# Optimization experiments

Hardware: AMD Instinct MI355X
Metric: run time of the kernel (lower is better)

Reference implementation:

```python
import jax, jax.numpy as jnp
import numpy as np

B, L, D, H, F, NL = 8, 1024, 640, 10, 1280, 6
DH = D // H
WINDOW = 64  # spatial-neighbor band half-width
NEG = -1e9


def layer_norm(x, g, b, eps=1e-5):
    m = jnp.mean(x, axis=-1, keepdims=True)
    v = jnp.mean((x - m) ** 2, axis=-1, keepdims=True)
    return (x - m) * jax.lax.rsqrt(v + eps) * g + b


def setup_inputs() -> dict:
    key = jax.random.key(0)
    ks = jax.random.split(key, 20)
    s = 0.02
    x = jax.random.normal(ks[0], (B, L, D), jnp.float32)
    y = jax.random.normal(ks[1], (B, L, D), jnp.float32)
    idx = jnp.arange(L)
    band = jnp.abs(idx[:, None] - idx[None, :]) > WINDOW  # True = disallowed
    x_attn_mask = jnp.broadcast_to(band, (B, L, L))
    y_attn_mask = jnp.broadcast_to(band, (B, L, L))
    x_pad_mask = jnp.zeros((B, L), bool)
    y_pad_mask = jnp.zeros((B, L), bool)
    # stacked per-layer encoder params (torch Linear convention: out = x @ W.T + b)
    params = dict(
        Wqkv=jax.random.normal(ks[2], (NL, 3 * D, D), jnp.float32) * s,
        bqkv=jnp.zeros((NL, 3 * D), jnp.float32),
        Wo=jax.random.normal(ks[3], (NL, D, D), jnp.float32) * s,
        bo=jnp.zeros((NL, D), jnp.float32),
        ln1_g=jnp.ones((NL, D), jnp.float32),
        ln1_b=jnp.zeros((NL, D), jnp.float32),
        W1=jax.random.normal(ks[4], (NL, F, D), jnp.float32) * s,
        b1=jnp.zeros((NL, F), jnp.float32),
        W2=jax.random.normal(ks[5], (NL, D, F), jnp.float32) * s,
        b2=jnp.zeros((NL, D), jnp.float32),
        ln2_g=jnp.ones((NL, D), jnp.float32),
        ln2_b=jnp.zeros((NL, D), jnp.float32),
        lne_g=jnp.ones((D,), jnp.float32),
        lne_b=jnp.zeros((D,), jnp.float32),
        We=jax.random.normal(ks[6], (D, D), jnp.float32) * s,
        be=jnp.zeros((D,), jnp.float32),
    )
    return dict(x=x, x_pad_mask=x_pad_mask, x_attn_mask=x_attn_mask,
                y=y, y_pad_mask=y_pad_mask, y_attn_mask=y_attn_mask, **params)


def _encoder(h, mask_bias, Wqkv, bqkv, Wo, bo, ln1_g, ln1_b, W1, b1, W2, b2, ln2_g, ln2_b):
    scale = 1.0 / np.sqrt(DH)

    def step(h, p):
        (wqkv, bq, wo, bo_, g1, be1, w1, bb1, w2, bb2, g2, be2) = p
        qkv = jnp.einsum('bld,ed->ble', h, wqkv) + bq
        q, k, v = jnp.split(qkv, 3, axis=-1)
        q = q.reshape(B, L, H, DH)
        k = k.reshape(B, L, H, DH)
        v = v.reshape(B, L, H, DH)
        scores = jnp.einsum('blhd,bmhd->bhlm', q, k) * scale + mask_bias  # (B,H,L,L)
        attn = jax.nn.softmax(scores, axis=-1)
        o = jnp.einsum('bhlm,bmhd->blhd', attn, v).reshape(B, L, D)
        o = jnp.einsum('bld,ed->ble', o, wo) + bo_
        h = layer_norm(h + o, g1, be1)  # post-LN (torch default norm_first=False)
        ff = jax.nn.relu(jnp.einsum('bld,fd->blf', h, w1) + bb1)
        ff = jnp.einsum('blf,df->bld', ff, w2) + bb2
        h = layer_norm(h + ff, g2, be2)
        return h, None

    ps = (Wqkv, bqkv, Wo, bo, ln1_g, ln1_b, W1, b1, W2, b2, ln2_g, ln2_b)
    h, _ = jax.lax.scan(step, h, ps)
    return h


def _embed_pool(x, pad_mask, attn_mask, P):
    # bool mask semantics (torch): True = not allowed to attend
    blocked = attn_mask | pad_mask[:, None, :]            # (B,L,L)
    mask_bias = jnp.where(blocked, NEG, 0.0)[:, None]      # (B,1,L,L), shared by heads
    h = _encoder(x, mask_bias, P['Wqkv'], P['bqkv'], P['Wo'], P['bo'],
                 P['ln1_g'], P['ln1_b'], P['W1'], P['b1'], P['W2'], P['b2'],
                 P['ln2_g'], P['ln2_b'])
    pooled = h.sum(axis=1)                                 # (B,D)
    e = layer_norm(pooled, P['lne_g'], P['lne_b'])
    return jax.nn.relu(e @ P['We'].T + P['be'])


def reference(x, x_pad_mask, x_attn_mask, y, y_pad_mask, y_attn_mask,
              Wqkv, bqkv, Wo, bo, ln1_g, ln1_b, W1, b1, W2, b2, ln2_g, ln2_b,
              lne_g, lne_b, We, be):
    P = dict(Wqkv=Wqkv, bqkv=bqkv, Wo=Wo, bo=bo, ln1_g=ln1_g, ln1_b=ln1_b,
             W1=W1, b1=b1, W2=W2, b2=b2, ln2_g=ln2_g, ln2_b=ln2_b,
             lne_g=lne_g, lne_b=lne_b, We=We, be=be)
    ex = _embed_pool(x, x_pad_mask, x_attn_mask, P)
    ey = _embed_pool(y, y_pad_mask, y_attn_mask, P)
    eps = 1e-8
    nx = jnp.maximum(jnp.linalg.norm(ex, axis=-1), eps)
    ny = jnp.maximum(jnp.linalg.norm(ey, axis=-1), eps)
    return jnp.sum(ex * ey, axis=-1) / (nx * ny)  # (B,)
```

## Files before the change

kernel.cpp:

```cpp
#include <hip/hip_runtime.h>


#define LSEQ   1024
#define DMODEL 640
#define NHEAD  10
#define DHEAD  64
#define NLAYER 6
#define BDIM   8
#define FDIM   1280
#define MROWS  (BDIM * LSEQ)

typedef __attribute__((ext_vector_type(8))) _Float16 half8;
typedef __attribute__((ext_vector_type(4))) _Float16 half4;
typedef __attribute__((ext_vector_type(2))) _Float16 half2v;
typedef __attribute__((ext_vector_type(4))) float    floatx4;
typedef __attribute__((ext_vector_type(2))) float    floatx2;

template <bool RELU, bool RESADD, bool SPLITK>
__global__ __launch_bounds__(256) void gemm_bt(const _Float16* __restrict__ A,
                                               const _Float16* __restrict__ Bw,
                                               const float* __restrict__ bias,
                                               const _Float16* __restrict__ res,
                                               _Float16* __restrict__ Cout,
                                               int M, int N, int K, int ld) {
  __shared__ _Float16 As[2][2][128 * 32];
  __shared__ _Float16 Bs[2][2][128 * 32];
  const int m0 = blockIdx.x * 128, n0 = blockIdx.y * 128;
  const int kz = SPLITK ? blockIdx.z : 0;
  const int tid = threadIdx.x;
  const int w = tid >> 6, lane = tid & 63;
  const int quad = lane >> 4, l16 = lane & 15;
  const int wm = w >> 1, wn = w & 1;

  floatx4 acc[4][4];
#pragma unroll
  for (int i = 0; i < 4; i++)
#pragma unroll
    for (int j = 0; j < 4; j++) acc[i][j] = (floatx4){0.f, 0.f, 0.f, 0.f};

  const int arow = w * 16 + (lane >> 2);
  const int kswz = ((lane & 3) ^ ((lane >> 3) & 3)) * 8;
  const _Float16* ag = A + (size_t)(m0 + arow) * ld + kz * K + kswz;
  const _Float16* bg = Bw + (size_t)(n0 + arow) * ld + kz * K + kswz;
  const size_t r64 = (size_t)64 * ld;
  const int wofs0 = arow * 32 + (lane & 3) * 8;
  const int wofs1 = wofs0 + 64 * 32;

  const int fro = l16 * 32 + ((quad ^ ((l16 >> 1) & 3)) * 8);

  const int nIter = K >> 6;
  {
    uint4 a00 = *(const uint4*)ag;
    uint4 a01 = *(const uint4*)(ag + r64);
    uint4 a10 = *(const uint4*)(ag + 32);
    uint4 a11 = *(const uint4*)(ag + 32 + r64);
    uint4 b00 = *(const uint4*)bg;
    uint4 b01 = *(const uint4*)(bg + r64);
    uint4 b10 = *(const uint4*)(bg + 32);
    uint4 b11 = *(const uint4*)(bg + 32 + r64);
    ag += 64; bg += 64;
    *(uint4*)&As[0][0][wofs0] = a00;
    *(uint4*)&As[0][0][wofs1] = a01;
    *(uint4*)&As[0][1][wofs0] = a10;
    *(uint4*)&As[0][1][wofs1] = a11;
    *(uint4*)&Bs[0][0][wofs0] = b00;
    *(uint4*)&Bs[0][0][wofs1] = b01;
    *(uint4*)&Bs[0][1][wofs0] = b10;
    *(uint4*)&Bs[0][1][wofs1] = b11;
  }

  for (int i = 0; i < nIter; i++) {
    __syncthreads();
    uint4 a00, a01, a10, a11, b00, b01, b10, b11;
    const bool pf = (i + 1 < nIter);
    if (pf) {
      a00 = *(const uint4*)ag;
      a01 = *(const uint4*)(ag + r64);
      a10 = *(const uint4*)(ag + 32);
      a11 = *(const uint4*)(ag + 32 + r64);
      b00 = *(const uint4*)bg;
      b01 = *(const uint4*)(bg + r64);
      b10 = *(const uint4*)(bg + 32);
      b11 = *(const uint4*)(bg + 32 + r64);
      ag += 64; bg += 64;
    }
#pragma unroll
    for (int sub = 0; sub < 2; sub++) {
      const _Float16* as = As[i & 1][sub];
      const _Float16* bs = Bs[i & 1][sub];
      half8 af[4], bf[4];
#pragma unroll
      for (int mt = 0; mt < 4; mt++)
        af[mt] = *(const half8*)&as[(wm * 64 + mt * 16) * 32 + fro];
#pragma unroll
      for (int nt = 0; nt < 4; nt++)
        bf[nt] = *(const half8*)&bs[(wn * 64 + nt * 16) * 32 + fro];
#pragma unroll
      for (int mt = 0; mt < 4; mt++)
#pragma unroll
        for (int nt = 0; nt < 4; nt++)
          acc[mt][nt] = __builtin_amdgcn_mfma_f32_16x16x32_f16(af[mt], bf[nt], acc[mt][nt], 0, 0, 0);
    }
    if (pf) {
      const int nb = (i + 1) & 1;
      *(uint4*)&As[nb][0][wofs0] = a00;
      *(uint4*)&As[nb][0][wofs1] = a01;
      *(uint4*)&As[nb][1][wofs0] = a10;
      *(uint4*)&As[nb][1][wofs1] = a11;
      *(uint4*)&Bs[nb][0][wofs0] = b00;
      *(uint4*)&Bs[nb][0][wofs1] = b01;
      *(uint4*)&Bs[nb][1][wofs0] = b10;
      *(uint4*)&Bs[nb][1][wofs1] = b11;
    }
  }

  const bool lead = (!SPLITK) || (kz == 0);
  _Float16* outp = Cout + (SPLITK ? (size_t)kz * ((size_t)M * N) : 0);
  float bv[4];
#pragma unroll
  for (int nt = 0; nt < 4; nt++)
    bv[nt] = lead ? bias[n0 + wn * 64 + nt * 16 + l16] : 0.f;
#pragma unroll
  for (int mt = 0; mt < 4; mt++) {
#pragma unroll
    for (int reg = 0; reg < 4; reg++) {
      const int row = m0 + wm * 64 + mt * 16 + quad * 4 + reg;
#pragma unroll
      for (int nt = 0; nt < 4; nt++) {
        const int col = n0 + wn * 64 + nt * 16 + l16;
        float v = acc[mt][nt][reg] + bv[nt];
        if (RESADD) { if (lead) v += (float)res[(size_t)row * N + col]; }
        if (RELU) v = fmaxf(v, 0.f);
        outp[(size_t)row * N + col] = (_Float16)v;
      }
    }
  }
}

__global__ __launch_bounds__(256) void attn_kernel(const _Float16* __restrict__ qkv,
                                                   _Float16* __restrict__ o) {
  __shared__ _Float16 Qs[64 * 72];
  __shared__ _Float16 KP[192 * 72];
  __shared__ _Float16 Vt[64 * 200];
  const int qb = blockIdx.x, h = blockIdx.y, b = blockIdx.z;
  const int q0 = qb * 64;
  const int kc0 = (q0 - 64 > 0) ? q0 - 64 : 0;
  const int kend = (q0 + 128 < LSEQ) ? q0 + 128 : LSEQ;
  const int cnt = kend - kc0;
  const int tid = threadIdx.x;

  for (int c = tid; c < 512; c += 256) {
    const int row = c >> 3, ch = c & 7;
    *(uint4*)&Qs[row * 72 + ch * 8] =
        *(const uint4*)(qkv + (size_t)(b * LSEQ + q0 + row) * (3 * DMODEL) + h * DHEAD + ch * 8);
  }
  for (int c = tid; c < 1536; c += 256) {
    const int row = c >> 3, ch = c & 7;
    uint4 v = {0u, 0u, 0u, 0u};
    if (row < cnt)
      v = *(const uint4*)(qkv + (size_t)(b * LSEQ + kc0 + row) * (3 * DMODEL) + DMODEL + h * DHEAD + ch * 8);
    *(uint4*)&KP[row * 72 + ch * 8] = v;
  }
  for (int c = tid; c < 1536; c += 256) {
    const int row = c >> 3, ch = c & 7;
    uint4 v = {0u, 0u, 0u, 0u};
    if (row < cnt)
      v = *(const uint4*)(qkv + (size_t)(b * LSEQ + kc0 + row) * (3 * DMODEL) + 2 * DMODEL + h * DHEAD + ch * 8);
    _Float16 tmp[8];
    *(uint4*)tmp = v;
    const int rs = row ^ (ch << 3);
#pragma unroll
    for (int jj = 0; jj < 8; jj++) Vt[(ch * 8 + jj) * 200 + rs] = tmp[jj];
  }
  __syncthreads();

  const int w = tid >> 6, lane = tid & 63, quad = lane >> 4, l16 = lane & 15;

  floatx4 sacc[12];
#pragma unroll
  for (int i = 0; i < 12; i++) sacc[i] = (floatx4){0.f, 0.f, 0.f, 0.f};
#pragma unroll
  for (int ks = 0; ks < 2; ks++) {
    const half8 qf = *(const half8*)&Qs[(w * 16 + l16) * 72 + ks * 32 + quad * 8];
#pragma unroll
    for (int nt = 0; nt < 12; nt++) {
      const half8 kf = *(const half8*)&KP[(nt * 16 + l16) * 72 + ks * 32 + quad * 8];
      sacc[nt] = __builtin_amdgcn_mfma_f32_16x16x32_f16(qf, kf, sacc[nt], 0, 0, 0);
    }
  }
  __syncthreads();

#pragma unroll
  for (int r = 0; r < 4; r++) {
    const int qi = q0 + w * 16 + quad * 4 + r;
    float sv[12];
    float m = -1e30f;
#pragma unroll
    for (int nt = 0; nt < 12; nt++) {
      const int key = kc0 + nt * 16 + l16;
      const bool ok = (key >= qi - 64) && (key <= qi + 64) && (key < LSEQ);
      const float s = ok ? sacc[nt][r] * 0.125f : -1e30f;
      sv[nt] = s;
      m = fmaxf(m, s);
    }
#pragma unroll
    for (int d = 1; d < 16; d <<= 1) m = fmaxf(m, __shfl_xor(m, d));
    float sum = 0.f;
#pragma unroll
    for (int nt = 0; nt < 12; nt++) {
      const float p = __expf(sv[nt] - m);
      sv[nt] = p;
      sum += p;
    }
#pragma unroll
    for (int d = 1; d < 16; d <<= 1) sum += __shfl_xor(sum, d);
    const float inv = 1.f / sum;
    _Float16* Pr = &KP[(w * 16 + quad * 4 + r) * 200];
#pragma unroll
    for (int nt = 0; nt < 12; nt++) Pr[nt * 16 + l16] = (_Float16)(sv[nt] * inv);
  }
  __syncthreads();

  floatx4 oacc[4];
#pragma unroll
  for (int i = 0; i < 4; i++) oacc[i] = (floatx4){0.f, 0.f, 0.f, 0.f};
#pragma unroll
  for (int ks = 0; ks < 6; ks++) {
    const half8 pf = *(const half8*)&KP[(w * 16 + l16) * 200 + ks * 32 + quad * 8];
#pragma unroll
    for (int nt = 0; nt < 4; nt++) {
      const int dsw = ((nt * 2 + (l16 >> 3)) & 7) << 3;
      const half8 vf = *(const half8*)&Vt[(nt * 16 + l16) * 200 + ((ks * 32 + quad * 8) ^ dsw)];
      oacc[nt] = __builtin_amdgcn_mfma_f32_16x16x32_f16(pf, vf, oacc[nt], 0, 0, 0);
    }
  }
#pragma unroll
  for (int nt = 0; nt < 4; nt++)
#pragma unroll
    for (int reg = 0; reg < 4; reg++) {
      const int row = q0 + w * 16 + quad * 4 + reg;
      const int col = h * DHEAD + nt * 16 + l16;
      o[(size_t)(b * LSEQ + row) * DMODEL + col] = (_Float16)oacc[nt][reg];
    }
}

__global__ __launch_bounds__(256) void ln_res2_kernel(const _Float16* __restrict__ s0,
                                                      const _Float16* __restrict__ s1,
                                                      const float* __restrict__ g,
                                                      const float* __restrict__ bta,
                                                      _Float16* __restrict__ hh) {
  const int row = blockIdx.x * 4 + (threadIdx.x >> 6);
  const int lane = threadIdx.x & 63;
  const _Float16* p0 = s0 + (size_t)row * DMODEL;
  const _Float16* p1 = s1 + (size_t)row * DMODEL;
  const half4  a0 = *(const half4*)(p0 + lane * 4);
  const half4  a1 = *(const half4*)(p0 + 256 + lane * 4);
  const half2v a2 = *(const half2v*)(p0 + 512 + lane * 2);
  const half4  c0 = *(const half4*)(p1 + lane * 4);
  const half4  c1 = *(const half4*)(p1 + 256 + lane * 4);
  const half2v c2 = *(const half2v*)(p1 + 512 + lane * 2);
  float v[10], s = 0.f, ss = 0.f;
#pragma unroll
  for (int j = 0; j < 4; j++) v[j] = (float)a0[j] + (float)c0[j];
#pragma unroll
  for (int j = 0; j < 4; j++) v[4 + j] = (float)a1[j] + (float)c1[j];
#pragma unroll
  for (int j = 0; j < 2; j++) v[8 + j] = (float)a2[j] + (float)c2[j];
#pragma unroll
  for (int i = 0; i < 10; i++) { s += v[i]; ss += v[i] * v[i]; }
#pragma unroll
  for (int d = 1; d < 64; d <<= 1) { s += __shfl_xor(s, d); ss += __shfl_xor(ss, d); }
  const float mean = s * (1.f / DMODEL);
  const float var = ss * (1.f / DMODEL) - mean * mean;
  const float rstd = rsqrtf(var + 1e-5f);
  const floatx4 g0 = *(const floatx4*)(g + lane * 4);
  const floatx4 g1 = *(const floatx4*)(g + 256 + lane * 4);
  const floatx2 g2 = *(const floatx2*)(g + 512 + lane * 2);
  const floatx4 b0 = *(const floatx4*)(bta + lane * 4);
  const floatx4 b1 = *(const floatx4*)(bta + 256 + lane * 4);
  const floatx2 b2 = *(const floatx2*)(bta + 512 + lane * 2);
  _Float16* outp = hh + (size_t)row * DMODEL;
  half4 o0, o1;
  half2v o2;
#pragma unroll
  for (int j = 0; j < 4; j++) o0[j] = (_Float16)((v[j] - mean) * rstd * g0[j] + b0[j]);
#pragma unroll
  for (int j = 0; j < 4; j++) o1[j] = (_Float16)((v[4 + j] - mean) * rstd * g1[j] + b1[j]);
#pragma unroll
  for (int j = 0; j < 2; j++) o2[j] = (_Float16)((v[8 + j] - mean) * rstd * g2[j] + b2[j]);
  *(half4*)(outp + lane * 4) = o0;
  *(half4*)(outp + 256 + lane * 4) = o1;
  *(half2v*)(outp + 512 + lane * 2) = o2;
}

__global__ void cvt_kernel(const float* __restrict__ s, _Float16* __restrict__ d, int n) {
  int i = blockIdx.x * blockDim.x + threadIdx.x;
  const int stride = gridDim.x * blockDim.x;
  for (; i < n; i += stride) d[i] = (_Float16)s[i];
}

__global__ void zero_kernel(float* __restrict__ p, int n) {
  const int i = blockIdx.x * blockDim.x + threadIdx.x;
  if (i < n) p[i] = 0.f;
}

__global__ void pool_kernel(const _Float16* __restrict__ h, float* __restrict__ pooled) {
  const int b = blockIdx.x, chunk = blockIdx.y;
  for (int d = threadIdx.x; d < DMODEL; d += 256) {
    float s = 0.f;
    const _Float16* p = h + ((size_t)b * LSEQ + chunk * 32) * DMODEL + d;
#pragma unroll 4
    for (int l = 0; l < 32; l++) s += (float)p[(size_t)l * DMODEL];
    atomicAdd(&pooled[b * DMODEL + d], s);
  }
}

__global__ void lnvec_kernel(const float* __restrict__ pooled, const float* __restrict__ g,
                             const float* __restrict__ bta, float* __restrict__ eln) {
  const int b = blockIdx.x, lane = threadIdx.x;
  float v[10], s = 0.f, ss = 0.f;
#pragma unroll
  for (int i = 0; i < 10; i++) {
    const float x = pooled[b * DMODEL + lane + 64 * i];
    v[i] = x; s += x; ss += x * x;
  }
#pragma unroll
  for (int d = 1; d < 64; d <<= 1) { s += __shfl_xor(s, d); ss += __shfl_xor(ss, d); }
  const float mean = s * (1.f / DMODEL);
  const float var = ss * (1.f / DMODEL) - mean * mean;
  const float rstd = rsqrtf(var + 1e-5f);
#pragma unroll
  for (int i = 0; i < 10; i++) {
    const int d = lane + 64 * i;
    eln[b * DMODEL + d] = (v[i] - mean) * rstd * g[d] + bta[d];
  }
}

__global__ __launch_bounds__(256) void embed_kernel(const float* __restrict__ eln,
                                                    const float* __restrict__ We,
                                                    const float* __restrict__ be,
                                                    float* __restrict__ e) {
  const int gw = (blockIdx.x << 2) + (threadIdx.x >> 6);
  const int lane = threadIdx.x & 63;
  const int b = gw / DMODEL, n = gw % DMODEL;
  const float* wr = We + (size_t)n * DMODEL;
  const float* er = eln + (size_t)b * DMODEL;
  float s = 0.f;
#pragma unroll
  for (int i = 0; i < 10; i++) s += wr[lane + 64 * i] * er[lane + 64 * i];
#pragma unroll
  for (int d = 1; d < 64; d <<= 1) s += __shfl_xor(s, d);
  if (lane == 0) e[(size_t)b * DMODEL + n] = fmaxf(s + be[n], 0.f);
}

__global__ void cosine_kernel(const float* __restrict__ ex, const float* __restrict__ ey,
                              float* __restrict__ out) {
  const int b = blockIdx.x, lane = threadIdx.x;
  float sxy = 0.f, sxx = 0.f, syy = 0.f;
#pragma unroll
  for (int i = 0; i < 10; i++) {
    const float x = ex[b * DMODEL + lane + 64 * i];
    const float y = ey[b * DMODEL + lane + 64 * i];
    sxy += x * y; sxx += x * x; syy += y * y;
  }
#pragma unroll
  for (int d = 1; d < 64; d <<= 1) {
    sxy += __shfl_xor(sxy, d); sxx += __shfl_xor(sxx, d); syy += __shfl_xor(syy, d);
  }
  if (lane == 0) {
    const float nx = fmaxf(sqrtf(sxx), 1e-8f);
    const float ny = fmaxf(sqrtf(syy), 1e-8f);
    out[b] = sxy / (nx * ny);
  }
}


extern "C" void kernel_launch(void* const* d_in, const int* in_sizes, int n_in,
                              void* d_out, int out_size, void* d_ws, size_t ws_size,
                              hipStream_t stream) {
  (void)in_sizes; (void)n_in; (void)out_size;
  const float* x    = (const float*)d_in[0];
  const float* y    = (const float*)d_in[3];
  const float* Wqkv = (const float*)d_in[6];
  const float* bqkv = (const float*)d_in[7];
  const float* Wo   = (const float*)d_in[8];
  const float* bo   = (const float*)d_in[9];
  const float* ln1g = (const float*)d_in[10];
  const float* ln1b = (const float*)d_in[11];
  const float* W1   = (const float*)d_in[12];
  const float* b1   = (const float*)d_in[13];
  const float* W2   = (const float*)d_in[14];
  const float* b2   = (const float*)d_in[15];
  const float* ln2g = (const float*)d_in[16];
  const float* ln2b = (const float*)d_in[17];
  const float* lneg = (const float*)d_in[18];
  const float* lneb = (const float*)d_in[19];
  const float* We   = (const float*)d_in[20];
  const float* be   = (const float*)d_in[21];

  auto algn = [](size_t b) { return (b + 255) & ~(size_t)255; };
  const size_t wbytes = algn((size_t)NLAYER * 3 * DMODEL * DMODEL * 2) +
                        algn((size_t)NLAYER * DMODEL * DMODEL * 2) +
                        2 * algn((size_t)NLAYER * FDIM * DMODEL * 2);
  auto actbytes = [&](size_t R) {
    return algn(R * DMODEL * 2) + algn(R * 3 * DMODEL * 2) + algn(R * FDIM * 2) +
           4 * algn((size_t)BDIM * DMODEL * 4);
  };
  const int NS = (wbytes + actbytes((size_t)2 * MROWS) <= ws_size) ? 2 : 1;
  const size_t R = (size_t)NS * MROWS;

  char* ws = (char*)d_ws;
  size_t off = 0;
  auto alloc = [&](size_t bytes) -> char* {
    char* p = ws + off;
    off += algn(bytes);
    return p;
  };
  _Float16* Wqkv_h = (_Float16*)alloc((size_t)NLAYER * 3 * DMODEL * DMODEL * 2);
  _Float16* Wo_h   = (_Float16*)alloc((size_t)NLAYER * DMODEL * DMODEL * 2);
  _Float16* W1_h   = (_Float16*)alloc((size_t)NLAYER * FDIM * DMODEL * 2);
  _Float16* W2_h   = (_Float16*)alloc((size_t)NLAYER * DMODEL * FDIM * 2);
  _Float16* h_h    = (_Float16*)alloc(R * DMODEL * 2);
  _Float16* qkv_h  = (_Float16*)alloc(R * 3 * DMODEL * 2);
  _Float16* ff_h   = (_Float16*)alloc(R * FDIM * 2);
  float*    pooled = (float*)   alloc((size_t)BDIM * DMODEL * 4);
  float*    elnb   = (float*)   alloc((size_t)BDIM * DMODEL * 4);
  float*    exb    = (float*)   alloc((size_t)BDIM * DMODEL * 4);
  float*    eyb    = (float*)   alloc((size_t)BDIM * DMODEL * 4);
  if (off > ws_size) return;
  _Float16* tmp2 = qkv_h;
  _Float16* o_h  = ff_h;

  cvt_kernel<<<2048, 256, 0, stream>>>(Wqkv, Wqkv_h, NLAYER * 3 * DMODEL * DMODEL);
  cvt_kernel<<<2048, 256, 0, stream>>>(Wo,   Wo_h,   NLAYER * DMODEL * DMODEL);
  cvt_kernel<<<2048, 256, 0, stream>>>(W1,   W1_h,   NLAYER * FDIM * DMODEL);
  cvt_kernel<<<2048, 256, 0, stream>>>(W2,   W2_h,   NLAYER * DMODEL * FDIM);

  const float* seq_in[2] = {x, y};
  float* eouts[2] = {exb, eyb};
  const int Mr = (int)R;
  const size_t halfo = (size_t)Mr * DMODEL;

  for (int s0 = 0; s0 < 2; s0 += NS) {
    for (int s = 0; s < NS; s++)
      cvt_kernel<<<2048, 256, 0, stream>>>(
          seq_in[s0 + s], h_h + (size_t)s * MROWS * DMODEL, MROWS * DMODEL);
    for (int l = 0; l < NLAYER; l++) {
      gemm_bt<false, false, false><<<dim3(Mr / 128, 15), 256, 0, stream>>>(
          h_h, Wqkv_h + (size_t)l * 3 * DMODEL * DMODEL, bqkv + l * 3 * DMODEL,
          nullptr, qkv_h, Mr, 3 * DMODEL, DMODEL, DMODEL);
      attn_kernel<<<dim3(LSEQ / 64, NHEAD, Mr / LSEQ), 256, 0, stream>>>(qkv_h, o_h);
      gemm_bt<false, true, true><<<dim3(Mr / 128, 5, 2), 256, 0, stream>>>(
          o_h, Wo_h + (size_t)l * DMODEL * DMODEL, bo + l * DMODEL,
          h_h, tmp2, Mr, DMODEL, DMODEL / 2, DMODEL);
      ln_res2_kernel<<<Mr / 4, 256, 0, stream>>>(
          tmp2, tmp2 + halfo, ln1g + l * DMODEL, ln1b + l * DMODEL, h_h);
      gemm_bt<true, false, false><<<dim3(Mr / 128, 10), 256, 0, stream>>>(
          h_h, W1_h + (size_t)l * FDIM * DMODEL, b1 + l * FDIM,
          nullptr, ff_h, Mr, FDIM, DMODEL, DMODEL);
      gemm_bt<false, true, true><<<dim3(Mr / 128, 5, 2), 256, 0, stream>>>(
          ff_h, W2_h + (size_t)l * DMODEL * FDIM, b2 + l * DMODEL,
          h_h, tmp2, Mr, DMODEL, FDIM / 2, FDIM);
      ln_res2_kernel<<<Mr / 4, 256, 0, stream>>>(
          tmp2, tmp2 + halfo, ln2g + l * DMODEL, ln2b + l * DMODEL, h_h);
    }
    for (int s = 0; s < NS; s++) {
      const _Float16* hseq = h_h + (size_t)s * MROWS * DMODEL;
      zero_kernel<<<(BDIM * DMODEL + 255) / 256, 256, 0, stream>>>(pooled, BDIM * DMODEL);
      pool_kernel<<<dim3(BDIM, 32), 256, 0, stream>>>(hseq, pooled);
      lnvec_kernel<<<BDIM, 64, 0, stream>>>(pooled, lneg, lneb, elnb);
      embed_kernel<<<BDIM * DMODEL / 4, 256, 0, stream>>>(elnb, We, be, eouts[s0 + s]);
    }
  }
  cosine_kernel<<<BDIM, 64, 0, stream>>>(exb, eyb, (float*)d_out);
}
```

Before: 1.836 ms.

## Use 256x256-tile 8-wave GEMM with direct global-to-LDS loads for QKV projection

Adds a new GEMM kernel that computes 256x256 output tiles with 512 threads, staging operands through global_load_lds directly into swizzled LDS with double buffering and setprio around MFMA blocks. It is used only for the QKV projection (N=1920, which needs column guarding since 1920 is not a multiple of 256). The larger tile raises arithmetic intensity and cuts global traffic per FLOP. In exchange the grid shrinks to 64x8 blocks, the last column tile wastes work, and the larger LDS footprint limits occupancy.

```diff
diff --git a/kernel.cpp b/kernel.cpp
--- a/kernel.cpp
+++ b/kernel.cpp
@@ -15,6 +15,172 @@
 typedef __attribute__((ext_vector_type(2))) _Float16 half2v;
 typedef __attribute__((ext_vector_type(4))) float    floatx4;
 typedef __attribute__((ext_vector_type(2))) float    floatx2;
+
+template <bool NGUARD>
+__global__ __launch_bounds__(512) void gemm_bt256p(const _Float16* __restrict__ A,
+                                                   const _Float16* __restrict__ Bw,
+                                                   const float* __restrict__ bias,
+                                                   _Float16* __restrict__ Cout,
+                                                   int M, int N, int K, int ld) {
+  __shared__ _Float16 As[2][2][256 * 32];
+  __shared__ _Float16 Bs[2][2][256 * 32];
+  const int m0 = blockIdx.x * 256, n0 = blockIdx.y * 256;
+  const int tid = threadIdx.x;
+  const int w = tid >> 6, lane = tid & 63;
+  const int quad = lane >> 4, l16 = lane & 15;
+  const int wm = w >> 2, wn = w & 3;
+
+  floatx4 acc[8][4];
+#pragma unroll
+  for (int i = 0; i < 8; i++)
+#pragma unroll
+    for (int j = 0; j < 4; j++) acc[i][j] = (floatx4){0.f, 0.f, 0.f, 0.f};
+
+  const int srow = w * 32 + (lane >> 2);
+  const int gswz = ((lane & 3) ^ ((lane >> 3) & 3)) * 8;
+  int br0 = n0 + srow, br1 = n0 + srow + 16;
+  if (NGUARD) { br0 = br0 < N - 1 ? br0 : N - 1; br1 = br1 < N - 1 ? br1 : N - 1; }
+  const _Float16* ag  = A + (size_t)(m0 + srow) * ld + gswz;
+  const _Float16* ag2 = ag + (size_t)16 * ld;
+  const _Float16* bg  = Bw + (size_t)br0 * ld + gswz;
+  const _Float16* bg2 = Bw + (size_t)br1 * ld + gswz;
+
+  typedef const __attribute__((address_space(1))) unsigned GU;
+  typedef __attribute__((address_space(3))) unsigned LU;
+  const int lbase = w * 1024;
+
+  auto issueH = [&](int col, int buf, int sub) {
+    _Float16* la = &As[buf][sub][lbase];
+    _Float16* lb = &Bs[buf][sub][lbase];
+    __builtin_amdgcn_global_load_lds((GU*)(ag  + col), (LU*)la,         16, 0, 0);
+    __builtin_amdgcn_global_load_lds((GU*)(ag2 + col), (LU*)(la + 512), 16, 0, 0);
+    __builtin_amdgcn_global_load_lds((GU*)(bg  + col), (LU*)lb,         16, 0, 0);
+    __builtin_amdgcn_global_load_lds((GU*)(bg2 + col), (LU*)(lb + 512), 16, 0, 0);
+  };
+
+  const int fro = l16 * 32 + ((quad ^ ((l16 >> 1) & 3)) * 8);
+
+  const int nt_ = K >> 6;
+
+  issueH(0, 0, 0);
+  issueH(32, 0, 1);
+  asm volatile("s_waitcnt vmcnt(4)" ::: "memory");
+  __builtin_amdgcn_s_barrier();
+
+  for (int t = 0; t < nt_; ++t) {
+    const int b = t & 1;
+    const bool pf = (t + 1 < nt_);
+    const int ncol = (t + 1) * 64;
+    half8 bf[4];
+    {
+      const _Float16* as = As[b][0];
+      const _Float16* bs = Bs[b][0];
+      half8 af[4];
+#pragma unroll
+      for (int mt = 0; mt < 4; mt++)
+        af[mt] = *(const half8*)&as[(wm * 128 + mt * 16) * 32 + fro];
+#pragma unroll
+      for (int n = 0; n < 4; n++)
+        bf[n] = *(const half8*)&bs[(wn * 64 + n * 16) * 32 + fro];
+      if (pf) issueH(ncol, b ^ 1, 0);
+      __builtin_amdgcn_s_barrier();
+      asm volatile("s_waitcnt lgkmcnt(0)" ::: "memory");
+      __builtin_amdgcn_sched_barrier(0);
+      __builtin_amdgcn_s_setprio(1);
+#pragma unroll
+      for (int mt = 0; mt < 4; mt++)
+#pragma unroll
+        for (int n = 0; n < 4; n++)
+          acc[mt][n] = __builtin_amdgcn_mfma_f32_16x16x32_f16(af[mt], bf[n], acc[mt][n], 0, 0, 0);
+      __builtin_amdgcn_s_setprio(0);
+      __builtin_amdgcn_s_barrier();
+    }
+    {
+      const _Float16* as = As[b][0];
+      half8 af[4];
+#pragma unroll
+      for (int mt = 0; mt < 4; mt++)
+        af[mt] = *(const half8*)&as[(wm * 128 + (4 + mt) * 16) * 32 + fro];
+      if (pf) issueH(ncol + 32, b ^ 1, 1);
+      __builtin_amdgcn_s_barrier();
+      asm volatile("s_waitcnt lgkmcnt(0)" ::: "memory");
+      __builtin_amdgcn_sched_barrier(0);
+      __builtin_amdgcn_s_setprio(1);
+#pragma unroll
+      for (int mt = 0; mt < 4; mt++)
+#pragma unroll
+        for (int n = 0; n < 4; n++)
+          acc[4 + mt][n] = __builtin_amdgcn_mfma_f32_16x16x32_f16(af[mt], bf[n], acc[4 + mt][n], 0, 0, 0);
+      __builtin_amdgcn_s_setprio(0);
+      if (pf) asm volatile("s_waitcnt vmcnt(8)" ::: "memory");
+      else    asm volatile("s_waitcnt vmcnt(0)" ::: "memory");
+      __builtin_amdgcn_s_barrier();
+    }
+    {
+      const _Float16* as = As[b][1];
+      const _Float16* bs = Bs[b][1];
+      half8 af[4];
+#pragma unroll
+      for (int mt = 0; mt < 4; mt++)
+        af[mt] = *(const half8*)&as[(wm * 128 + mt * 16) * 32 + fro];
+#pragma unroll
+      for (int n = 0; n < 4; n++)
+        bf[n] = *(const half8*)&bs[(wn * 64 + n * 16) * 32 + fro];
+      __builtin_amdgcn_s_barrier();
+      asm volatile("s_waitcnt lgkmcnt(0)" ::: "memory");
+      __builtin_amdgcn_sched_barrier(0);
+      __builtin_amdgcn_s_setprio(1);
+#pragma unroll
+      for (int mt = 0; mt < 4; mt++)
+#pragma unroll
+        for (int n = 0; n < 4; n++)
+          acc[mt][n] = __builtin_amdgcn_mfma_f32_16x16x32_f16(af[mt], bf[n], acc[mt][n], 0, 0, 0);
+      __builtin_amdgcn_s_setprio(0);
+      __builtin_amdgcn_s_barrier();
+    }
+    {
+      const _Float16* as = As[b][1];
+      half8 af[4];
+#pragma unroll
+      for (int mt = 0; mt < 4; mt++)
+        af[mt] = *(const half8*)&as[(wm * 128 + (4 + mt) * 16) * 32 + fro];
+      __builtin_amdgcn_s_barrier();
+      asm volatile("s_waitcnt lgkmcnt(0)" ::: "memory");
+      __builtin_amdgcn_sched_barrier(0);
+      __builtin_amdgcn_s_setprio(1);
+#pragma unroll
+      for (int mt = 0; mt < 4; mt++)
+#pragma unroll
+        for (int n = 0; n < 4; n++)
+          acc[4 + mt][n] = __builtin_amdgcn_mfma_f32_16x16x32_f16(af[mt], bf[n], acc[4 + mt][n], 0, 0, 0);
+      __builtin_amdgcn_s_setprio(0);
+      if (pf) asm volatile("s_waitcnt vmcnt(4)" ::: "memory");
+      __builtin_amdgcn_s_barrier();
+    }
+  }
+
+  float bv[4];
+#pragma unroll
+  for (int nt = 0; nt < 4; nt++) {
+    int c = n0 + wn * 64 + nt * 16 + l16;
+    if (NGUARD) c = c < N - 1 ? c : N - 1;
+    bv[nt] = bias[c];
+  }
+#pragma unroll
+  for (int mt = 0; mt < 8; mt++) {
+#pragma unroll
+    for (int reg = 0; reg < 4; reg++) {
+      const int row = m0 + wm * 128 + mt * 16 + quad * 4 + reg;
+#pragma unroll
+      for (int nt = 0; nt < 4; nt++) {
+        const int col = n0 + wn * 64 + nt * 16 + l16;
+        if (NGUARD && col >= N) continue;
+        float v = acc[mt][nt][reg] + bv[nt];
+        Cout[(size_t)row * N + col] = (_Float16)v;
+      }
+    }
+  }
+}
 
 template <bool RELU, bool RESADD, bool SPLITK>
 __global__ __launch_bounds__(256) void gemm_bt(const _Float16* __restrict__ A,
@@ -446,9 +612,9 @@
       cvt_kernel<<<2048, 256, 0, stream>>>(
           seq_in[s0 + s], h_h + (size_t)s * MROWS * DMODEL, MROWS * DMODEL);
     for (int l = 0; l < NLAYER; l++) {
-      gemm_bt<false, false, false><<<dim3(Mr / 128, 15), 256, 0, stream>>>(
+      gemm_bt256p<true><<<dim3(Mr / 256, 8), 512, 0, stream>>>(
           h_h, Wqkv_h + (size_t)l * 3 * DMODEL * DMODEL, bqkv + l * 3 * DMODEL,
-          nullptr, qkv_h, Mr, 3 * DMODEL, DMODEL, DMODEL);
+          qkv_h, Mr, 3 * DMODEL, DMODEL, DMODEL);
       attn_kernel<<<dim3(LSEQ / 64, NHEAD, Mr / LSEQ), 256, 0, stream>>>(qkv_h, o_h);
       gemm_bt<false, true, true><<<dim3(Mr / 128, 5, 2), 256, 0, stream>>>(
           o_h, Wo_h + (size_t)l * DMODEL * DMODEL, bo + l * DMODEL,
```

Measured after the change: 1.945 ms. +5.9%, slower.
